# Performance work log

Hardware: AMD Instinct MI355X
Metric: run time of the kernel (lower is better)

## Reference

```python
import jax, jax.numpy as jnp
import numpy as np

FG_THRESH = 0.5

def _descriptors(fmap, scribbles):
    # fmap: [B, C, h, w]; scribbles: [B, I, H, W]
    B, C, h, w = fmap.shape
    I = scribbles.shape[1]
    # bilinear resize (align_corners=False == half-pixel, no antialias, like torch)
    sr = jax.image.resize(scribbles, (B, I, h, w), method='bilinear', antialias=False)
    mask = (sr > FG_THRESH).astype(fmap.dtype)                 # [B, I, h, w]
    cnt = mask.sum(axis=(-1, -2))                              # [B, I]
    ssum = jnp.einsum('bihw,bchw->bic', mask, fmap)            # masked sum over HW
    mean = ssum / jnp.maximum(cnt, 1.0)[..., None]             # [B, I, C]
    # fallback when a mask has no foreground pixels: feature at argmax of soft mask
    idx = jnp.argmax(sr.reshape(B, I, h * w), axis=-1)         # [B, I]
    fflat = fmap.reshape(B, C, h * w)
    fb = jnp.take_along_axis(fflat, idx[:, None, :], axis=2)   # [B, C, I]
    fb = fb.transpose(0, 2, 1)                                 # [B, I, C]
    return jnp.where((cnt > 0)[..., None], mean, fb)

def setup_inputs() -> dict:
    key = jax.random.key(0)
    k0, k1, k2, k3 = jax.random.split(key, 4)
    return {
        'feat0': jax.random.normal(k0, (8, 256, 128, 128), dtype=jnp.float32),
        'feat1': jax.random.normal(k1, (8, 256, 64, 64), dtype=jnp.float32),
        'feat2': jax.random.normal(k2, (8, 256, 32, 32), dtype=jnp.float32),
        'scribbles': jax.random.uniform(k3, (8, 16, 512, 512), dtype=jnp.float32),
    }

def reference(feat0, feat1, feat2, scribbles):
    # multi_scale=True, random_bg_queries=False: per-level masked mean pool,
    # then average descriptors across feature levels. Output: [B, I, C]
    d0 = _descriptors(feat0, scribbles)
    d1 = _descriptors(feat1, scribbles)
    d2 = _descriptors(feat2, scribbles)
    return (d0 + d1 + d2) / 3.0
```

## Files before the change

### kernel.cpp

```cpp
#include <hip/hip_runtime.h>
#include <stdint.h>

#define NB 8
#define NI 16
#define NC 256
#define SH 512
#define NCH 168

typedef __bf16 bf16x8 __attribute__((ext_vector_type(8)));
typedef float f32x4 __attribute__((ext_vector_type(4)));
typedef uint32_t u32x4 __attribute__((ext_vector_type(4)));

static const size_t OFF_SSP = 0;
static const size_t OFF_CNT = OFF_SSP + (size_t)NB * NCH * NI * NC * 4;
static const size_t OFF_KEY = OFF_CNT + (size_t)NB * NCH * NI * 4;
static const size_t WS_NEED = OFF_KEY + (size_t)NB * NCH * NI * 8;

__device__ __forceinline__ float4 ld4(const float* p) {
    return *reinterpret_cast<const float4*>(p);
}

template<int W, int S, int P>
__device__ __forceinline__ void do_chunk(const float* __restrict__ f,
                                         const float* __restrict__ scr,
                                         float* __restrict__ ssp,
                                         int* __restrict__ cntp,
                                         unsigned long long* __restrict__ keyp,
                                         int b, int chunk, int slot, int tid,
                                         uint8_t* __restrict__ lmask8,
                                         uint16_t* __restrict__ lmask16,
                                         int* __restrict__ lcnt,
                                         unsigned long long* __restrict__ lkey) {
    const int gi = tid >> 7;
    const int p = tid & 127;
    const int pix = chunk * 128 + p;
    const int y = pix / W;
    const int x = pix - y * W;
    const int r0 = S * y + (S / 2 - 1);
    const int c0s = S * x + (S / 2 - 1);
    const int lane = tid & 63;
    const float* sb = scr + ((size_t)b * NI + gi * 8) * (SH * SH) + (size_t)r0 * SH;
    unsigned int mword = 0;
    #pragma unroll
    for (int i = 0; i < 8; ++i) {
        const float* sp = sb + (size_t)i * (SH * SH);
        float s4;
        if constexpr (S == 4) {
            float4 q0 = ld4(sp + (c0s - 1));
            float4 q1 = ld4(sp + SH + (c0s - 1));
            s4 = (q0.y + q0.z) + (q1.y + q1.z);
        } else {
            s4 = (sp[c0s] + sp[c0s + 1]) + (sp[SH + c0s] + sp[SH + c0s + 1]);
        }
        bool bit = s4 > 2.0f;
        mword |= bit ? (1u << i) : 0u;
        unsigned long long bal = __ballot(bit);
        if (lane == 0) atomicAdd(&lcnt[gi * 8 + i], (int)__popcll(bal));
        if (bal == 0ull) {
            unsigned int srb = __float_as_uint(0.25f * s4);
            unsigned int mx = srb;
            #pragma unroll
            for (int off = 1; off < 64; off <<= 1) {
                unsigned int o = __shfl_xor(mx, off, 64);
                mx = (o > mx) ? o : mx;
            }
            unsigned long long win = __ballot(srb == mx);
            if (lane == 0) {
                int wl = __ffsll((unsigned long long)win) - 1;
                unsigned int wpix = (unsigned int)(chunk * 128 + (p & ~63) + wl);
                unsigned long long key = (((unsigned long long)mx) << 32)
                                       | (unsigned long long)(0xFFFFFFFFu - wpix);
                atomicMax(&lkey[gi * 8 + i], key);
            }
        }
    }
    lmask8[gi * 128 + p] = (uint8_t)mword;
    __syncthreads();
    if (tid < 128)
        lmask16[tid] = (uint16_t)(lmask8[tid] | ((unsigned)lmask8[128 + tid] << 8));
    if (tid < NI) {
        cntp[slot * NI + tid] = lcnt[tid];
        keyp[slot * NI + tid] = lkey[tid];
    }
    __syncthreads();

    const int wave = tid >> 6;
    const int kg = lane >> 4;
    const int cl = lane & 15;
    const int c0 = wave * 64;
    const int kb = chunk * 128;
    const uint16_t* lmp = lmask16 + kg * 8;
    const float* fp0 = f + ((size_t)b * NC + c0 + cl) * P + kb + kg * 8;
    f32x4 acc0 = {0.f, 0.f, 0.f, 0.f};
    f32x4 acc1 = {0.f, 0.f, 0.f, 0.f};
    f32x4 acc2 = {0.f, 0.f, 0.f, 0.f};
    f32x4 acc3 = {0.f, 0.f, 0.f, 0.f};
    #pragma unroll
    for (int ks = 0; ks < 4; ++ks) {
        const uint4 wA = *reinterpret_cast<const uint4*>(lmp + ks * 32);
        u32x4 au;
        au.x = ((wA.x >> cl) & 0x10001u) * 0x3F80u;
        au.y = ((wA.y >> cl) & 0x10001u) * 0x3F80u;
        au.z = ((wA.z >> cl) & 0x10001u) * 0x3F80u;
        au.w = ((wA.w >> cl) & 0x10001u) * 0x3F80u;
        const bf16x8 av = __builtin_bit_cast(bf16x8, au);
        const float* fk = fp0 + ks * 32;
        #pragma unroll
        for (int nt = 0; nt < 4; ++nt) {
            const float* fr = fk + (size_t)(nt * 16) * P;
            float4 v0 = ld4(fr);
            float4 v1 = ld4(fr + 4);
            bf16x8 bv;
            bv[0] = (__bf16)v0.x; bv[1] = (__bf16)v0.y;
            bv[2] = (__bf16)v0.z; bv[3] = (__bf16)v0.w;
            bv[4] = (__bf16)v1.x; bv[5] = (__bf16)v1.y;
            bv[6] = (__bf16)v1.z; bv[7] = (__bf16)v1.w;
            if (nt == 0) acc0 = __builtin_amdgcn_mfma_f32_16x16x32_bf16(av, bv, acc0, 0, 0, 0);
            if (nt == 1) acc1 = __builtin_amdgcn_mfma_f32_16x16x32_bf16(av, bv, acc1, 0, 0, 0);
            if (nt == 2) acc2 = __builtin_amdgcn_mfma_f32_16x16x32_bf16(av, bv, acc2, 0, 0, 0);
            if (nt == 3) acc3 = __builtin_amdgcn_mfma_f32_16x16x32_bf16(av, bv, acc3, 0, 0, 0);
        }
    }
    float* sb2 = ssp + (size_t)slot * (NI * NC);
    #pragma unroll
    for (int nt = 0; nt < 4; ++nt) {
        const f32x4 ac = (nt == 0) ? acc0 : (nt == 1) ? acc1 : (nt == 2) ? acc2 : acc3;
        const int c = c0 + nt * 16 + cl;
        #pragma unroll
        for (int r = 0; r < 4; ++r)
            sb2[(kg * 4 + r) * NC + c] = ac[r];
    }
}

__global__ __launch_bounds__(256) void fused_kernel(const float* __restrict__ f0,
                                                    const float* __restrict__ f1,
                                                    const float* __restrict__ f2,
                                                    const float* __restrict__ scr,
                                                    float* __restrict__ ssp,
                                                    int* __restrict__ cntp,
                                                    unsigned long long* __restrict__ keyp) {
    __shared__ uint8_t lmask8[256];
    __shared__ __align__(16) uint16_t lmask16[128];
    __shared__ int lcnt[NI];
    __shared__ unsigned long long lkey[NI];
    const int tid = threadIdx.x;
    const int b = blockIdx.y;
    const int bx = blockIdx.x;
    if (tid < NI) { lcnt[tid] = 0; lkey[tid] = 0ull; }
    __syncthreads();
    const int slot = b * NCH + bx;
    if (bx < 128) {
        do_chunk<128, 4, 16384>(f0, scr, ssp, cntp, keyp, b, bx, slot, tid,
                                lmask8, lmask16, lcnt, lkey);
    } else if (bx < 160) {
        do_chunk<64, 8, 4096>(f1, scr, ssp, cntp, keyp, b, bx - 128, slot, tid,
                              lmask8, lmask16, lcnt, lkey);
    } else {
        do_chunk<32, 16, 1024>(f2, scr, ssp, cntp, keyp, b, bx - 160, slot, tid,
                               lmask8, lmask16, lcnt, lkey);
    }
}

__global__ __launch_bounds__(256) void final_kernel(const float* __restrict__ f0,
                                                    const float* __restrict__ f1,
                                                    const float* __restrict__ f2,
                                                    const int* __restrict__ cntp,
                                                    const unsigned long long* __restrict__ keyp,
                                                    const float* __restrict__ ssp,
                                                    float* __restrict__ out) {
    __shared__ int scnt[3];
    __shared__ unsigned long long skey[3];
    __shared__ float red[4][64];
    const int bi = blockIdx.x;
    const int cq = blockIdx.y;
    const int b = bi >> 4;
    const int i = bi & 15;
    const int tid = threadIdx.x;
    const int cl = tid & 63;
    const int jg = tid >> 6;
    const int CH[3] = {128, 32, 8};
    const int O[3] = {0, 128, 160};
    if (tid < 3) { scnt[tid] = 0; skey[tid] = 0ull; }
    __syncthreads();
    if (tid < NCH) {
        int l = (tid < 128) ? 0 : (tid < 160) ? 1 : 2;
        const int slot = b * NCH + tid;
        atomicAdd(&scnt[l], cntp[slot * NI + i]);
        atomicMax(&skey[l], keyp[slot * NI + i]);
    }
    __syncthreads();
    const float* fl[3] = {f0, f1, f2};
    const int Ps[3] = {16384, 4096, 1024};
    float r = 0.f;
    #pragma unroll
    for (int l = 0; l < 3; ++l) {
        const int cn = scnt[l];
        if (cn > 0) {
            float s = 0.f;
            for (int j = jg; j < CH[l]; j += 4)
                s += ssp[((size_t)(b * NCH + O[l] + j) * NI + i) * NC + cq * 64 + cl];
            red[jg][cl] = s;
            __syncthreads();
            if (jg == 0)
                r += ((red[0][cl] + red[1][cl]) + (red[2][cl] + red[3][cl])) / (float)cn;
            __syncthreads();
        } else if (jg == 0) {
            unsigned int p = 0xFFFFFFFFu - (unsigned int)(skey[l] & 0xFFFFFFFFull);
            r += fl[l][((size_t)b * NC + cq * 64 + cl) * Ps[l] + p];
        }
    }
    if (jg == 0) out[(size_t)bi * NC + cq * 64 + cl] = r * (1.f / 3.f);
}

extern "C" void kernel_launch(void* const* d_in, const int* in_sizes, int n_in,
                              void* d_out, int out_size, void* d_ws, size_t ws_size,
                              hipStream_t stream) {
    const float* f0  = (const float*)d_in[0];
    const float* f1  = (const float*)d_in[1];
    const float* f2  = (const float*)d_in[2];
    const float* scr = (const float*)d_in[3];
    float* out = (float*)d_out;
    char* ws = (char*)d_ws;
    if (ws_size < WS_NEED) return;

    float* ssp = (float*)(ws + OFF_SSP);
    int* cntp = (int*)(ws + OFF_CNT);
    unsigned long long* keyp = (unsigned long long*)(ws + OFF_KEY);

    fused_kernel<<<dim3(NCH, NB), 256, 0, stream>>>(f0, f1, f2, scr, ssp, cntp, keyp);
    final_kernel<<<dim3(NB * NI, 4), 256, 0, stream>>>(f0, f1, f2, cntp, keyp, ssp, out);
}
```

Baseline: 75.42 us.

## Double chunk size to 256 pixels and software-pipeline feature loads with MFMA

```diff
diff --git a/kernel.cpp b/kernel.cpp
--- a/kernel.cpp
+++ b/kernel.cpp
@@ -5,7 +5,7 @@
 #define NI 16
 #define NC 256
 #define SH 512
-#define NCH 168
+#define NCH 84
 
 typedef __bf16 bf16x8 __attribute__((ext_vector_type(8)));
 typedef float f32x4 __attribute__((ext_vector_type(4)));
@@ -18,6 +18,28 @@
 
 __device__ __forceinline__ float4 ld4(const float* p) {
     return *reinterpret_cast<const float4*>(p);
+}
+
+__device__ __forceinline__ void mfma_step(const uint16_t* __restrict__ lmp, int ks, int cl,
+                                          const float4 (&buf)[4][2],
+                                          f32x4& a0, f32x4& a1, f32x4& a2, f32x4& a3) {
+    const uint4 wA = *reinterpret_cast<const uint4*>(lmp + ks * 32);
+    u32x4 au;
+    au.x = ((wA.x >> cl) & 0x10001u) * 0x3F80u;
+    au.y = ((wA.y >> cl) & 0x10001u) * 0x3F80u;
+    au.z = ((wA.z >> cl) & 0x10001u) * 0x3F80u;
+    au.w = ((wA.w >> cl) & 0x10001u) * 0x3F80u;
+    const bf16x8 av = __builtin_bit_cast(bf16x8, au);
+    #pragma unroll
+    for (int nt = 0; nt < 4; ++nt) {
+        bf16x8 bv;
+        bv[0] = (__bf16)buf[nt][0].x; bv[1] = (__bf16)buf[nt][0].y;
+        bv[2] = (__bf16)buf[nt][0].z; bv[3] = (__bf16)buf[nt][0].w;
+        bv[4] = (__bf16)buf[nt][1].x; bv[5] = (__bf16)buf[nt][1].y;
+        bv[6] = (__bf16)buf[nt][1].z; bv[7] = (__bf16)buf[nt][1].w;
+        f32x4& ac = (nt == 0) ? a0 : (nt == 1) ? a1 : (nt == 2) ? a2 : a3;
+        ac = __builtin_amdgcn_mfma_f32_16x16x32_bf16(av, bv, ac, 0, 0, 0);
+    }
 }
 
 template<int W, int S, int P>
@@ -27,22 +49,33 @@
                                          int* __restrict__ cntp,
                                          unsigned long long* __restrict__ keyp,
                                          int b, int chunk, int slot, int tid,
-                                         uint8_t* __restrict__ lmask8,
-                                         uint16_t* __restrict__ lmask16,
+                                         uint16_t* __restrict__ lmask,
                                          int* __restrict__ lcnt,
                                          unsigned long long* __restrict__ lkey) {
-    const int gi = tid >> 7;
-    const int p = tid & 127;
-    const int pix = chunk * 128 + p;
+    const int wave = tid >> 6;
+    const int lane = tid & 63;
+    const int kg = lane >> 4;
+    const int cl = lane & 15;
+    const int c0 = wave * 64;
+    const int kb = chunk * 256;
+    const float* fp0 = f + ((size_t)b * NC + c0 + cl) * P + kb + kg * 8;
+    float4 bA[4][2], bB[4][2];
+    #pragma unroll
+    for (int nt = 0; nt < 4; ++nt) {
+        const float* fr = fp0 + (size_t)(nt * 16) * P;
+        bA[nt][0] = ld4(fr);
+        bA[nt][1] = ld4(fr + 4);
+    }
+
+    const int pix = chunk * 256 + tid;
     const int y = pix / W;
     const int x = pix - y * W;
     const int r0 = S * y + (S / 2 - 1);
     const int c0s = S * x + (S / 2 - 1);
-    const int lane = tid & 63;
-    const float* sb = scr + ((size_t)b * NI + gi * 8) * (SH * SH) + (size_t)r0 * SH;
+    const float* sb = scr + (size_t)b * NI * (SH * SH) + (size_t)r0 * SH;
     unsigned int mword = 0;
     #pragma unroll
-    for (int i = 0; i < 8; ++i) {
+    for (int i = 0; i < NI; ++i) {
         const float* sp = sb + (size_t)i * (SH * SH);
         float s4;
         if constexpr (S == 4) {
@@ -55,7 +88,7 @@
         bool bit = s4 > 2.0f;
         mword |= bit ? (1u << i) : 0u;
         unsigned long long bal = __ballot(bit);
-        if (lane == 0) atomicAdd(&lcnt[gi * 8 + i], (int)__popcll(bal));
+        if (lane == 0) atomicAdd(&lcnt[i], (int)__popcll(bal));
         if (bal == 0ull) {
             unsigned int srb = __float_as_uint(0.25f * s4);
             unsigned int mx = srb;
@@ -67,59 +100,43 @@
             unsigned long long win = __ballot(srb == mx);
             if (lane == 0) {
                 int wl = __ffsll((unsigned long long)win) - 1;
-                unsigned int wpix = (unsigned int)(chunk * 128 + (p & ~63) + wl);
+                unsigned int wpix = (unsigned int)(chunk * 256 + (tid & ~63) + wl);
                 unsigned long long key = (((unsigned long long)mx) << 32)
                                        | (unsigned long long)(0xFFFFFFFFu - wpix);
-                atomicMax(&lkey[gi * 8 + i], key);
+                atomicMax(&lkey[i], key);
             }
         }
     }
-    lmask8[gi * 128 + p] = (uint8_t)mword;
-    __syncthreads();
-    if (tid < 128)
-        lmask16[tid] = (uint16_t)(lmask8[tid] | ((unsigned)lmask8[128 + tid] << 8));
+    lmask[tid] = (uint16_t)mword;
+    __syncthreads();
     if (tid < NI) {
         cntp[slot * NI + tid] = lcnt[tid];
         keyp[slot * NI + tid] = lkey[tid];
     }
-    __syncthreads();
-
-    const int wave = tid >> 6;
-    const int kg = lane >> 4;
-    const int cl = lane & 15;
-    const int c0 = wave * 64;
-    const int kb = chunk * 128;
-    const uint16_t* lmp = lmask16 + kg * 8;
-    const float* fp0 = f + ((size_t)b * NC + c0 + cl) * P + kb + kg * 8;
+
+    const uint16_t* lmp = lmask + kg * 8;
     f32x4 acc0 = {0.f, 0.f, 0.f, 0.f};
     f32x4 acc1 = {0.f, 0.f, 0.f, 0.f};
     f32x4 acc2 = {0.f, 0.f, 0.f, 0.f};
     f32x4 acc3 = {0.f, 0.f, 0.f, 0.f};
     #pragma unroll
-    for (int ks = 0; ks < 4; ++ks) {
-        const uint4 wA = *reinterpret_cast<const uint4*>(lmp + ks * 32);
-        u32x4 au;
-        au.x = ((wA.x >> cl) & 0x10001u) * 0x3F80u;
-        au.y = ((wA.y >> cl) & 0x10001u) * 0x3F80u;
-        au.z = ((wA.z >> cl) & 0x10001u) * 0x3F80u;
-        au.w = ((wA.w >> cl) & 0x10001u) * 0x3F80u;
-        const bf16x8 av = __builtin_bit_cast(bf16x8, au);
-        const float* fk = fp0 + ks * 32;
+    for (int ks = 0; ks < 8; ks += 2) {
         #pragma unroll
         for (int nt = 0; nt < 4; ++nt) {
-            const float* fr = fk + (size_t)(nt * 16) * P;
-            float4 v0 = ld4(fr);
-            float4 v1 = ld4(fr + 4);
-            bf16x8 bv;
-            bv[0] = (__bf16)v0.x; bv[1] = (__bf16)v0.y;
-            bv[2] = (__bf16)v0.z; bv[3] = (__bf16)v0.w;
-            bv[4] = (__bf16)v1.x; bv[5] = (__bf16)v1.y;
-            bv[6] = (__bf16)v1.z; bv[7] = (__bf16)v1.w;
-            if (nt == 0) acc0 = __builtin_amdgcn_mfma_f32_16x16x32_bf16(av, bv, acc0, 0, 0, 0);
-            if (nt == 1) acc1 = __builtin_amdgcn_mfma_f32_16x16x32_bf16(av, bv, acc1, 0, 0, 0);
-            if (nt == 2) acc2 = __builtin_amdgcn_mfma_f32_16x16x32_bf16(av, bv, acc2, 0, 0, 0);
-            if (nt == 3) acc3 = __builtin_amdgcn_mfma_f32_16x16x32_bf16(av, bv, acc3, 0, 0, 0);
-        }
+            const float* fr = fp0 + (size_t)(nt * 16) * P + (ks + 1) * 32;
+            bB[nt][0] = ld4(fr);
+            bB[nt][1] = ld4(fr + 4);
+        }
+        mfma_step(lmp, ks, cl, bA, acc0, acc1, acc2, acc3);
+        if (ks + 2 < 8) {
+            #pragma unroll
+            for (int nt = 0; nt < 4; ++nt) {
+                const float* fr = fp0 + (size_t)(nt * 16) * P + (ks + 2) * 32;
+                bA[nt][0] = ld4(fr);
+                bA[nt][1] = ld4(fr + 4);
+            }
+        }
+        mfma_step(lmp, ks + 1, cl, bB, acc0, acc1, acc2, acc3);
     }
     float* sb2 = ssp + (size_t)slot * (NI * NC);
     #pragma unroll
@@ -132,15 +149,14 @@
     }
 }
 
-__global__ __launch_bounds__(256) void fused_kernel(const float* __restrict__ f0,
-                                                    const float* __restrict__ f1,
-                                                    const float* __restrict__ f2,
-                                                    const float* __restrict__ scr,
-                                                    float* __restrict__ ssp,
-                                                    int* __restrict__ cntp,
-                                                    unsigned long long* __restrict__ keyp) {
-    __shared__ uint8_t lmask8[256];
-    __shared__ __align__(16) uint16_t lmask16[128];
+__global__ __launch_bounds__(256, 2) void fused_kernel(const float* __restrict__ f0,
+                                                       const float* __restrict__ f1,
+                                                       const float* __restrict__ f2,
+                                                       const float* __restrict__ scr,
+                                                       float* __restrict__ ssp,
+                                                       int* __restrict__ cntp,
+                                                       unsigned long long* __restrict__ keyp) {
+    __shared__ __align__(16) uint16_t lmask[256];
     __shared__ int lcnt[NI];
     __shared__ unsigned long long lkey[NI];
     const int tid = threadIdx.x;
@@ -149,15 +165,15 @@
     if (tid < NI) { lcnt[tid] = 0; lkey[tid] = 0ull; }
     __syncthreads();
     const int slot = b * NCH + bx;
-    if (bx < 128) {
+    if (bx < 64) {
         do_chunk<128, 4, 16384>(f0, scr, ssp, cntp, keyp, b, bx, slot, tid,
-                                lmask8, lmask16, lcnt, lkey);
-    } else if (bx < 160) {
-        do_chunk<64, 8, 4096>(f1, scr, ssp, cntp, keyp, b, bx - 128, slot, tid,
-                              lmask8, lmask16, lcnt, lkey);
+                                lmask, lcnt, lkey);
+    } else if (bx < 80) {
+        do_chunk<64, 8, 4096>(f1, scr, ssp, cntp, keyp, b, bx - 64, slot, tid,
+                              lmask, lcnt, lkey);
     } else {
-        do_chunk<32, 16, 1024>(f2, scr, ssp, cntp, keyp, b, bx - 160, slot, tid,
-                               lmask8, lmask16, lcnt, lkey);
+        do_chunk<32, 16, 1024>(f2, scr, ssp, cntp, keyp, b, bx - 80, slot, tid,
+                               lmask, lcnt, lkey);
     }
 }
 
@@ -178,12 +194,12 @@
     const int tid = threadIdx.x;
     const int cl = tid & 63;
     const int jg = tid >> 6;
-    const int CH[3] = {128, 32, 8};
-    const int O[3] = {0, 128, 160};
+    const int CH[3] = {64, 16, 4};
+    const int O[3] = {0, 64, 80};
     if (tid < 3) { scnt[tid] = 0; skey[tid] = 0ull; }
     __syncthreads();
     if (tid < NCH) {
-        int l = (tid < 128) ? 0 : (tid < 160) ? 1 : 2;
+        int l = (tid < 64) ? 0 : (tid < 80) ? 1 : 2;
         const int slot = b * NCH + tid;
         atomicAdd(&scnt[l], cntp[slot * NI + i]);
         atomicMax(&skey[l], keyp[slot * NI + i]);
```

After: 69.61 us. 1.08x faster.
